# Performance work log

Measured on AMD Instinct MI355X. Metric: run time of the kernel, lower is better.

The kernel has to match this reference:

```python
import jax, jax.numpy as jnp
import numpy as np

D_MODEL = 1024
D_HIDDEN = 4096
N_EXPERTS = 8
N_TOKENS = 4096


def setup_inputs() -> dict:
    key = jax.random.key(0)
    ks = jax.random.split(key, 7)
    s = 0.02
    return {
        "x": jax.random.normal(ks[0], (N_TOKENS, D_MODEL), dtype=jnp.float32),
        "gate_w": jax.random.normal(ks[1], (N_EXPERTS, D_MODEL), dtype=jnp.float32) * s,
        "gate_b": jnp.zeros((N_EXPERTS,), dtype=jnp.float32),
        "w1": jax.random.normal(ks[2], (N_EXPERTS, D_MODEL, D_HIDDEN), dtype=jnp.float32) * s,
        "b1": jnp.zeros((N_EXPERTS, D_HIDDEN), dtype=jnp.float32),
        "w2": jax.random.normal(ks[3], (N_EXPERTS, D_HIDDEN, D_MODEL), dtype=jnp.float32) * s,
        "b2": jnp.zeros((N_EXPERTS, D_MODEL), dtype=jnp.float32),
    }


def reference(x, gate_w, gate_b, w1, b1, w2, b2):
    # gate: softmax over expert logits, hard top-1 routing (no prob weighting,
    # matching the torch module which writes the raw expert output back)
    gate_logits = x @ gate_w.T + gate_b                      # [N, E]
    gate_probs = jax.nn.softmax(gate_logits, axis=-1)
    top_expert = jnp.argmax(gate_probs, axis=-1)             # [N] int

    # dense all-expert MLP, then one-hot select (vectorized top-1 MoE)
    h = jax.nn.relu(jnp.einsum('nd,edh->neh', x, w1) + b1[None])  # [N, E, Dh]
    y = jnp.einsum('neh,ehd->ned', h, w2) + b2[None]              # [N, E, D]
    onehot = jax.nn.one_hot(top_expert, N_EXPERTS, dtype=x.dtype)  # [N, E]
    out = jnp.einsum('ned,ne->nd', y, onehot)                      # [N, D]
    return out
```

## Files before the change

### kernel.cpp

```cpp
#include <hip/hip_runtime.h>
#include <hip/hip_bf16.h>

#define NT 4096
#define DM 1024
#define DH 4096
#define NE 8

#define BM 128
#define BN 128
#define BK 32
#define KSPLIT 4
#define BKP 40

typedef short bf16x8 __attribute__((ext_vector_type(8)));
typedef float f32x4 __attribute__((ext_vector_type(4)));

#define O_COUNTS 0ull
#define O_OFF    64ull
#define O_BUCKET 256ull
#define O_XB     (O_BUCKET + (size_t)NE * NT * 4)
#define O_H      (O_XB + (size_t)NT * DM * 2)
#define O_W1T    (O_H + (size_t)NT * DH * 2)
#define O_W2T    (O_W1T + (size_t)NE * DM * DH * 2)
#define WS_NEED  (O_W2T + (size_t)NE * DH * DM * 2)
#define O_P      O_W1T

static __device__ __forceinline__ unsigned short f2bf(float f) {
  union { __hip_bfloat16 h; unsigned short u; } cv;
  cv.h = __float2bfloat16(f);
  return cv.u;
}

static __device__ __forceinline__ void gload16(const void* g, void* l) {
  __builtin_amdgcn_global_load_lds(
      (const __attribute__((address_space(1))) void*)g,
      (__attribute__((address_space(3))) void*)l, 16, 0, 0);
}

__global__ __launch_bounds__(256) void gate_route_kernel(
    const float* __restrict__ x, const float* __restrict__ gw,
    const float* __restrict__ gb, int* __restrict__ counts,
    int* __restrict__ bucket, __hip_bfloat16* __restrict__ xb) {
  const int wid = threadIdx.x >> 6;
  const int lane = threadIdx.x & 63;
  const int t = blockIdx.x * 4 + wid;

  const float4* xrow = (const float4*)(x + (size_t)t * DM);
  ushort4* xbrow = (ushort4*)(xb + (size_t)t * DM);

  double part[NE];
#pragma unroll
  for (int e = 0; e < NE; ++e) part[e] = 0.0;

#pragma unroll
  for (int q = 0; q < 4; ++q) {
    float4 v = xrow[q * 64 + lane];
    ushort4 s;
    s.x = f2bf(v.x); s.y = f2bf(v.y); s.z = f2bf(v.z); s.w = f2bf(v.w);
    xbrow[q * 64 + lane] = s;
#pragma unroll
    for (int e = 0; e < NE; ++e) {
      float4 w = ((const float4*)(gw + (size_t)e * DM))[q * 64 + lane];
      part[e] += (double)v.x * w.x + (double)v.y * w.y +
                 (double)v.z * w.z + (double)v.w * w.w;
    }
  }
#pragma unroll
  for (int off = 32; off; off >>= 1) {
#pragma unroll
    for (int e = 0; e < NE; ++e) part[e] += __shfl_down(part[e], off);
  }
  if (lane == 0) {
    double best = part[0] + (double)gb[0];
    int bi = 0;
#pragma unroll
    for (int e = 1; e < NE; ++e) {
      double le = part[e] + (double)gb[e];
      if (le > best) { best = le; bi = e; }
    }
    int pos = atomicAdd(&counts[bi], 1);
    bucket[bi * NT + pos] = t;
  }
}

__global__ void prefix_kernel(const int* __restrict__ counts,
                              int* __restrict__ off) {
  if (threadIdx.x == 0 && blockIdx.x == 0) {
    int r = 0;
#pragma unroll
    for (int e = 0; e < NE; ++e) { off[e] = r; r += counts[e]; }
    off[NE] = r;
  }
}

__global__ __launch_bounds__(256) void convert_tr_kernel(
    const float* __restrict__ src, __hip_bfloat16* __restrict__ dst, int K,
    int N) {
  const int e = blockIdx.z;
  const int n0 = blockIdx.x * 64, k0 = blockIdx.y * 64;
  const float* S = src + (size_t)e * K * N;
  __hip_bfloat16* D = dst + (size_t)e * K * N;
  __shared__ __align__(16) __hip_bfloat16 Ls[64][72];
  const int tid = threadIdx.x;
  const int rk = tid >> 4, c4 = tid & 15;
#pragma unroll
  for (int j = 0; j < 4; ++j) {
    const int k = rk + 16 * j;
    float4 v = *(const float4*)(S + (size_t)(k0 + k) * N + n0 + c4 * 4);
    Ls[c4 * 4 + 0][k] = __float2bfloat16(v.x);
    Ls[c4 * 4 + 1][k] = __float2bfloat16(v.y);
    Ls[c4 * 4 + 2][k] = __float2bfloat16(v.z);
    Ls[c4 * 4 + 3][k] = __float2bfloat16(v.w);
  }
  __syncthreads();
  const int rn = tid >> 2, q = tid & 3;
#pragma unroll
  for (int j = 0; j < 2; ++j) {
    const int ch = q + 4 * j;
    uint4 w = *(const uint4*)&Ls[rn][ch * 8];
    *(uint4*)(D + (size_t)(n0 + rn) * K + k0 + ch * 8) = w;
  }
}

template <int MODE>
__global__ __launch_bounds__(256) void moe_gemm_fast(
    const __hip_bfloat16* __restrict__ A, const __hip_bfloat16* __restrict__ B,
    const float* __restrict__ biasAll, const int* __restrict__ counts,
    const int* __restrict__ off, const int* __restrict__ bucket,
    void* __restrict__ Out, int Ktot, int N, int lda) {
  const int e = blockIdx.z & (NE - 1);
  const int kq = blockIdx.z >> 3;
  const int cnt = counts[e];
  const int m0 = blockIdx.y * BM;
  if (m0 >= cnt) return;
  const int goff = off[e];
  const int n0 = blockIdx.x * BN;
  const int kbase = kq * (DH / KSPLIT);

  __shared__ __align__(16) __hip_bfloat16 As[BM][BK];
  __shared__ __align__(16) __hip_bfloat16 Bs[BN][BK];

  const int tid = threadIdx.x;
  const int lane = tid & 63;
  const int wid = tid >> 6;
  const int lr = lane >> 2, lc = lane & 3;

  const int s0 = min(m0 + 32 * wid + lr, cnt - 1);
  const int s1 = min(m0 + 32 * wid + 16 + lr, cnt - 1);
  const __hip_bfloat16 *aP0, *aP1;
  if (MODE == 0) {
    aP0 = A + (size_t)bucket[e * NT + s0] * lda + lc * 8;
    aP1 = A + (size_t)bucket[e * NT + s1] * lda + lc * 8;
  } else {
    aP0 = A + (size_t)(goff + s0) * lda + kbase + lc * 8;
    aP1 = A + (size_t)(goff + s1) * lda + kbase + lc * 8;
  }
  const __hip_bfloat16* bP0 =
      B + ((size_t)e * N + n0 + 32 * wid + lr) * Ktot + kbase + lc * 8;
  const __hip_bfloat16* bP1 = bP0 + (size_t)16 * Ktot;

  __hip_bfloat16* dA0 = &As[32 * wid][0];
  __hip_bfloat16* dA1 = &As[32 * wid + 16][0];
  __hip_bfloat16* dB0 = &Bs[32 * wid][0];
  __hip_bfloat16* dB1 = &Bs[32 * wid + 16][0];

  const int wm = (wid >> 1) * 64, wn = (wid & 1) * 64;
  const int fr = lane & 15, ks = lane >> 4;

  f32x4 acc[4][4];
#pragma unroll
  for (int m = 0; m < 4; ++m)
#pragma unroll
    for (int n = 0; n < 4; ++n) acc[m][n] = (f32x4){0.f, 0.f, 0.f, 0.f};

  for (int kt = 0; kt < 32; ++kt) {
    const int ko = kt * BK;
    gload16(aP0 + ko, dA0);
    gload16(aP1 + ko, dA1);
    gload16(bP0 + ko, dB0);
    gload16(bP1 + ko, dB1);
    __syncthreads();
    bf16x8 afr[4], bfr[4];
#pragma unroll
    for (int m = 0; m < 4; ++m)
      afr[m] = *(const bf16x8*)&As[wm + m * 16 + fr][ks * 8];
#pragma unroll
    for (int n = 0; n < 4; ++n)
      bfr[n] = *(const bf16x8*)&Bs[wn + n * 16 + fr][ks * 8];
#pragma unroll
    for (int m = 0; m < 4; ++m)
#pragma unroll
      for (int n = 0; n < 4; ++n)
        acc[m][n] = __builtin_amdgcn_mfma_f32_16x16x32_bf16(afr[m], bfr[n],
                                                            acc[m][n], 0, 0, 0);
    __syncthreads();
  }

  if (MODE == 0) {
    const float* bias = biasAll + (size_t)e * DH;
    __hip_bfloat16* Hout = (__hip_bfloat16*)Out;
#pragma unroll
    for (int m = 0; m < 4; ++m)
#pragma unroll
      for (int r = 0; r < 4; ++r) {
        const int slot = m0 + wm + m * 16 + ks * 4 + r;
        if (slot < cnt) {
          __hip_bfloat16* orow = Hout + (size_t)(goff + slot) * DH;
#pragma unroll
          for (int n = 0; n < 4; ++n) {
            const int col = n0 + wn + n * 16 + fr;
            float v = acc[m][n][r] + bias[col];
            orow[col] = __float2bfloat16(v > 0.f ? v : 0.f);
          }
        }
      }
  } else {
    float* Pout = (float*)Out + (size_t)kq * NT * DM;
#pragma unroll
    for (int m = 0; m < 4; ++m)
#pragma unroll
      for (int r = 0; r < 4; ++r) {
        const int slot = m0 + wm + m * 16 + ks * 4 + r;
        if (slot < cnt) {
          float* orow = Pout + (size_t)(goff + slot) * DM;
#pragma unroll
          for (int n = 0; n < 4; ++n) {
            const int col = n0 + wn + n * 16 + fr;
            orow[col] = acc[m][n][r];
          }
        }
      }
  }
}

__global__ __launch_bounds__(256) void reduce_out_kernel(
    const float* __restrict__ P, const float* __restrict__ b2,
    const int* __restrict__ off, const int* __restrict__ bucket,
    float* __restrict__ out) {
  const int gs = blockIdx.x;
  int e = 0;
#pragma unroll
  for (int i = 1; i < NE; ++i) e = (gs >= off[i]) ? i : e;
  const int tok = bucket[e * NT + (gs - off[e])];
  const int c = threadIdx.x * 4;
  float4 v = *(const float4*)(P + (size_t)gs * DM + c);
#pragma unroll
  for (int q = 1; q < KSPLIT; ++q) {
    float4 p = *(const float4*)(P + ((size_t)q * NT + gs) * DM + c);
    v.x += p.x; v.y += p.y; v.z += p.z; v.w += p.w;
  }
  float4 b = *(const float4*)(b2 + (size_t)e * DM + c);
  v.x += b.x; v.y += b.y; v.z += b.z; v.w += b.w;
  *(float4*)(out + (size_t)tok * DM + c) = v;
}

template <bool RELU_BF16>
__global__ __launch_bounds__(256, 2) void moe_gemm_fallback(
    const __hip_bfloat16* __restrict__ Aall, int lda,
    const float* __restrict__ Ball, int K, int N,
    const float* __restrict__ biasAll, const int* __restrict__ counts,
    const int* __restrict__ bucket, void* __restrict__ Out, int ldo) {
  const int e = blockIdx.z;
  const int cnt = counts[e];
  const int m0 = blockIdx.y * BM;
  if (m0 >= cnt) return;
  const int n0 = blockIdx.x * BN;

  const float* Bp = Ball + (size_t)e * K * N;
  const float* bias = biasAll + (size_t)e * N;
  const int* buck = bucket + e * NT;

  __shared__ __align__(16) __hip_bfloat16 As[2][BM][BKP];
  __shared__ __align__(16) __hip_bfloat16 Bs[2][BN][BKP];

  const int tid = threadIdx.x;
  const int lane = tid & 63;
  const int wid = tid >> 6;
  const int wm = (wid >> 1) * 64;
  const int wn = (wid & 1) * 64;
  const int fr = lane & 15;
  const int ks = lane >> 4;

  const int ar = tid >> 1;
  const int ah = tid & 1;
  const int atok = buck[min(m0 + ar, cnt - 1)];
  const __hip_bfloat16* aptr = Aall + (size_t)atok * lda + ah * 16;

  const int bc = tid & 31;
  const int bk0 = (tid >> 5) * 4;

  f32x4 acc[4][4];
#pragma unroll
  for (int m = 0; m < 4; ++m)
#pragma unroll
    for (int n = 0; n < 4; ++n) acc[m][n] = (f32x4){0.f, 0.f, 0.f, 0.f};

  const int KT = K / BK;
  uint4 ra0, ra1;
  float rb[4][4];

  {
    const uint4* p = (const uint4*)(aptr);
    ra0 = p[0]; ra1 = p[1];
    const float* bbase = Bp + (size_t)bk0 * N + n0 + bc;
#pragma unroll
    for (int i = 0; i < 4; ++i)
#pragma unroll
      for (int j = 0; j < 4; ++j) rb[i][j] = bbase[(size_t)i * N + 32 * j];
  }
  {
    *(uint4*)&As[0][ar][ah * 16] = ra0;
    *(uint4*)&As[0][ar][ah * 16 + 8] = ra1;
#pragma unroll
    for (int j = 0; j < 4; ++j) {
      ushort4 w;
      w.x = f2bf(rb[0][j]); w.y = f2bf(rb[1][j]);
      w.z = f2bf(rb[2][j]); w.w = f2bf(rb[3][j]);
      *(ushort4*)&Bs[0][bc + 32 * j][bk0] = w;
    }
  }
  __syncthreads();

  for (int kt = 0; kt < KT; ++kt) {
    const int buf = kt & 1;
    if (kt + 1 < KT) {
      const uint4* p = (const uint4*)(aptr + (size_t)(kt + 1) * BK);
      ra0 = p[0]; ra1 = p[1];
      const float* bbase = Bp + (size_t)((kt + 1) * BK + bk0) * N + n0 + bc;
#pragma unroll
      for (int i = 0; i < 4; ++i)
#pragma unroll
        for (int j = 0; j < 4; ++j) rb[i][j] = bbase[(size_t)i * N + 32 * j];
    }

    bf16x8 afr[4], bfr[4];
#pragma unroll
    for (int m = 0; m < 4; ++m)
      afr[m] = *(const bf16x8*)&As[buf][wm + m * 16 + fr][ks * 8];
#pragma unroll
    for (int n = 0; n < 4; ++n)
      bfr[n] = *(const bf16x8*)&Bs[buf][wn + n * 16 + fr][ks * 8];
#pragma unroll
    for (int m = 0; m < 4; ++m)
#pragma unroll
      for (int n = 0; n < 4; ++n)
        acc[m][n] = __builtin_amdgcn_mfma_f32_16x16x32_bf16(afr[m], bfr[n],
                                                            acc[m][n], 0, 0, 0);

    __syncthreads();
    if (kt + 1 < KT) {
      *(uint4*)&As[buf ^ 1][ar][ah * 16] = ra0;
      *(uint4*)&As[buf ^ 1][ar][ah * 16 + 8] = ra1;
#pragma unroll
      for (int j = 0; j < 4; ++j) {
        ushort4 w;
        w.x = f2bf(rb[0][j]); w.y = f2bf(rb[1][j]);
        w.z = f2bf(rb[2][j]); w.w = f2bf(rb[3][j]);
        *(ushort4*)&Bs[buf ^ 1][bc + 32 * j][bk0] = w;
      }
      __syncthreads();
    }
  }

  float* outF = (float*)Out;
  __hip_bfloat16* outB = (__hip_bfloat16*)Out;
#pragma unroll
  for (int m = 0; m < 4; ++m) {
#pragma unroll
    for (int r = 0; r < 4; ++r) {
      const int row = wm + m * 16 + ks * 4 + r;
      const int slot = m0 + row;
      if (slot < cnt) {
        const int tok = buck[slot];
#pragma unroll
        for (int n = 0; n < 4; ++n) {
          const int col = n0 + wn + n * 16 + fr;
          float v = acc[m][n][r] + bias[col];
          if (RELU_BF16) {
            v = v > 0.f ? v : 0.f;
            outB[(size_t)tok * ldo + col] = __float2bfloat16(v);
          } else {
            outF[(size_t)tok * ldo + col] = v;
          }
        }
      }
    }
  }
}

extern "C" void kernel_launch(void* const* d_in, const int* in_sizes, int n_in,
                              void* d_out, int out_size, void* d_ws,
                              size_t ws_size, hipStream_t stream) {
  const float* x = (const float*)d_in[0];
  const float* gw = (const float*)d_in[1];
  const float* gb = (const float*)d_in[2];
  const float* w1 = (const float*)d_in[3];
  const float* b1 = (const float*)d_in[4];
  const float* w2 = (const float*)d_in[5];
  const float* b2 = (const float*)d_in[6];
  (void)in_sizes; (void)n_in; (void)out_size;

  char* ws = (char*)d_ws;
  int* counts = (int*)(ws + O_COUNTS);
  int* off = (int*)(ws + O_OFF);
  int* bucket = (int*)(ws + O_BUCKET);
  __hip_bfloat16* xb = (__hip_bfloat16*)(ws + O_XB);
  __hip_bfloat16* h = (__hip_bfloat16*)(ws + O_H);

  hipMemsetAsync(ws, 0, 256, stream);
  gate_route_kernel<<<NT / 4, 256, 0, stream>>>(x, gw, gb, counts, bucket, xb);

  if (ws_size >= WS_NEED) {
    __hip_bfloat16* w1t = (__hip_bfloat16*)(ws + O_W1T);
    __hip_bfloat16* w2t = (__hip_bfloat16*)(ws + O_W2T);
    float* P = (float*)(ws + O_P);

    prefix_kernel<<<1, 64, 0, stream>>>(counts, off);
    convert_tr_kernel<<<dim3(DH / 64, DM / 64, NE), 256, 0, stream>>>(
        w1, w1t, DM, DH);
    moe_gemm_fast<0><<<dim3(DH / BN, NT / BM, NE), 256, 0, stream>>>(
        xb, w1t, b1, counts, off, bucket, (void*)h, DM, DH, DM);
    convert_tr_kernel<<<dim3(DM / 64, DH / 64, NE), 256, 0, stream>>>(
        w2, w2t, DH, DM);
    moe_gemm_fast<1><<<dim3(DM / BN, NT / BM, NE * KSPLIT), 256, 0, stream>>>(
        h, w2t, nullptr, counts, off, bucket, (void*)P, DH, DM, DH);
    reduce_out_kernel<<<NT, 256, 0, stream>>>(P, b2, off, bucket,
                                              (float*)d_out);
  } else {
    dim3 g1(DH / BN, NT / BM, NE);
    moe_gemm_fallback<true><<<g1, 256, 0, stream>>>(
        xb, DM, w1, DM, DH, b1, counts, bucket, (void*)h, DH);
    dim3 g2(DM / BN, NT / BM, NE);
    moe_gemm_fallback<false><<<g2, 256, 0, stream>>>(
        h, DH, w2, DH, DM, b2, counts, bucket, d_out, DM);
  }
}
```

Measured before the change: 304.0 us.

## Double-buffer LDS tiles and flatten grid with expert-fastest block order

Adds a two-stage LDS ring so the next K-tile's global loads are issued before computing on the current tile, leaving one barrier per iteration. The 3D grid becomes a 1D grid where the expert index varies fastest and the M tile next, so neighbouring blocks cover different experts and early-exit blocks are spread across the launch. Double buffering doubles LDS use per block, which can lower occupancy, and gains depend on whether gload16 is asynchronous enough to overlap with the MFMAs.

```diff
diff --git a/kernel.cpp b/kernel.cpp
--- a/kernel.cpp
+++ b/kernel.cpp
@@ -9,6 +9,7 @@
 #define BM 128
 #define BN 128
 #define BK 32
+#define NMT (NT / BM)
 #define KSPLIT 4
 #define BKP 40
 
@@ -128,17 +129,24 @@
     const float* __restrict__ biasAll, const int* __restrict__ counts,
     const int* __restrict__ off, const int* __restrict__ bucket,
     void* __restrict__ Out, int Ktot, int N, int lda) {
-  const int e = blockIdx.z & (NE - 1);
-  const int kq = blockIdx.z >> 3;
+  int flat = blockIdx.x;
+  const int e = flat & (NE - 1);
+  int t = flat >> 3;
+  const int mtile = t % NMT;
+  t /= NMT;
+  int kq, ntile;
+  if (MODE == 0) { kq = 0; ntile = t; }
+  else { kq = t % KSPLIT; ntile = t / KSPLIT; }
+
   const int cnt = counts[e];
-  const int m0 = blockIdx.y * BM;
+  const int m0 = mtile * BM;
   if (m0 >= cnt) return;
   const int goff = off[e];
-  const int n0 = blockIdx.x * BN;
+  const int n0 = ntile * BN;
   const int kbase = kq * (DH / KSPLIT);
 
-  __shared__ __align__(16) __hip_bfloat16 As[BM][BK];
-  __shared__ __align__(16) __hip_bfloat16 Bs[BN][BK];
+  __shared__ __align__(16) __hip_bfloat16 As[2][BM][BK];
+  __shared__ __align__(16) __hip_bfloat16 Bs[2][BN][BK];
 
   const int tid = threadIdx.x;
   const int lane = tid & 63;
@@ -159,11 +167,6 @@
       B + ((size_t)e * N + n0 + 32 * wid + lr) * Ktot + kbase + lc * 8;
   const __hip_bfloat16* bP1 = bP0 + (size_t)16 * Ktot;
 
-  __hip_bfloat16* dA0 = &As[32 * wid][0];
-  __hip_bfloat16* dA1 = &As[32 * wid + 16][0];
-  __hip_bfloat16* dB0 = &Bs[32 * wid][0];
-  __hip_bfloat16* dB1 = &Bs[32 * wid + 16][0];
-
   const int wm = (wid >> 1) * 64, wn = (wid & 1) * 64;
   const int fr = lane & 15, ks = lane >> 4;
 
@@ -173,20 +176,28 @@
 #pragma unroll
     for (int n = 0; n < 4; ++n) acc[m][n] = (f32x4){0.f, 0.f, 0.f, 0.f};
 
+#define STAGE(buf, kt)                                \
+  do {                                                \
+    const int ko_ = (kt) * BK;                        \
+    gload16(aP0 + ko_, &As[buf][32 * wid][0]);        \
+    gload16(aP1 + ko_, &As[buf][32 * wid + 16][0]);   \
+    gload16(bP0 + ko_, &Bs[buf][32 * wid][0]);        \
+    gload16(bP1 + ko_, &Bs[buf][32 * wid + 16][0]);   \
+  } while (0)
+
+  STAGE(0, 0);
+  __syncthreads();
+
   for (int kt = 0; kt < 32; ++kt) {
-    const int ko = kt * BK;
-    gload16(aP0 + ko, dA0);
-    gload16(aP1 + ko, dA1);
-    gload16(bP0 + ko, dB0);
-    gload16(bP1 + ko, dB1);
-    __syncthreads();
+    const int buf = kt & 1;
+    if (kt + 1 < 32) STAGE(buf ^ 1, kt + 1);
     bf16x8 afr[4], bfr[4];
 #pragma unroll
     for (int m = 0; m < 4; ++m)
-      afr[m] = *(const bf16x8*)&As[wm + m * 16 + fr][ks * 8];
+      afr[m] = *(const bf16x8*)&As[buf][wm + m * 16 + fr][ks * 8];
 #pragma unroll
     for (int n = 0; n < 4; ++n)
-      bfr[n] = *(const bf16x8*)&Bs[wn + n * 16 + fr][ks * 8];
+      bfr[n] = *(const bf16x8*)&Bs[buf][wn + n * 16 + fr][ks * 8];
 #pragma unroll
     for (int m = 0; m < 4; ++m)
 #pragma unroll
@@ -195,6 +206,7 @@
                                                             acc[m][n], 0, 0, 0);
     __syncthreads();
   }
+#undef STAGE
 
   if (MODE == 0) {
     const float* bias = biasAll + (size_t)e * DH;
@@ -418,11 +430,11 @@
     prefix_kernel<<<1, 64, 0, stream>>>(counts, off);
     convert_tr_kernel<<<dim3(DH / 64, DM / 64, NE), 256, 0, stream>>>(
         w1, w1t, DM, DH);
-    moe_gemm_fast<0><<<dim3(DH / BN, NT / BM, NE), 256, 0, stream>>>(
+    moe_gemm_fast<0><<<NE * NMT * (DH / BN), 256, 0, stream>>>(
         xb, w1t, b1, counts, off, bucket, (void*)h, DM, DH, DM);
     convert_tr_kernel<<<dim3(DM / 64, DH / 64, NE), 256, 0, stream>>>(
         w2, w2t, DH, DM);
-    moe_gemm_fast<1><<<dim3(DM / BN, NT / BM, NE * KSPLIT), 256, 0, stream>>>(
+    moe_gemm_fast<1><<<NE * NMT * KSPLIT * (DM / BN), 256, 0, stream>>>(
         h, w2t, nullptr, counts, off, bucket, (void*)P, DH, DM, DH);
     reduce_out_kernel<<<NT, 256, 0, stream>>>(P, b2, off, bucket,
                                               (float*)d_out);
```

Result: slower. 320.7 us (+5.5%).
